# Optimization experiments

Measured on AMD Instinct MI355X. Metric: run time of the kernel, lower is better.

## Reference

```python
import jax, jax.numpy as jnp
import numpy as np

TIME_SCALE = 10.0
EPS = 1e-5


def _ln(x, g, b):
    m = jnp.mean(x, axis=-1, keepdims=True)
    v = jnp.mean((x - m) ** 2, axis=-1, keepdims=True)
    return (x - m) * jax.lax.rsqrt(v + EPS) * g + b


def setup_inputs() -> dict:
    key = jax.random.key(0)
    ks = jax.random.split(key, 16)
    B, S, D, H, C = 128, 2048, 67, 256, 1

    def lin(k, fan_in, shape):
        return (jax.random.uniform(k, shape, jnp.float32) * 2.0 - 1.0) / np.sqrt(fan_in)

    inp = {
        "x": jax.random.normal(ks[0], (B, S, D), jnp.float32),
        "dt": jax.random.uniform(ks[1], (B, S, 1), jnp.float32),
        # input LayerNorm
        "ln_in_g": jnp.ones((D,), jnp.float32),
        "ln_in_b": jnp.zeros((D,), jnp.float32),
        # feature projection: Linear(D,H) + LayerNorm(H) (+SiLU)
        "proj_W": lin(ks[2], D, (D, H)),
        "proj_b": jnp.zeros((H,), jnp.float32),
        "ln_p_g": jnp.ones((H,), jnp.float32),
        "ln_p_b": jnp.zeros((H,), jnp.float32),
        # CfC cell: four linears from concat([x_t, h]) (2H -> H)
        "W_ff1": lin(ks[3], 2 * H, (2 * H, H)),
        "b_ff1": jnp.zeros((H,), jnp.float32),
        "W_ff2": lin(ks[4], 2 * H, (2 * H, H)),
        "b_ff2": jnp.zeros((H,), jnp.float32),
        "W_ta": lin(ks[5], 2 * H, (2 * H, H)),
        "b_ta": jnp.zeros((H,), jnp.float32),
        "W_tb": lin(ks[6], 2 * H, (2 * H, H)),
        "b_tb": jnp.zeros((H,), jnp.float32),
        # event head: LayerNorm(H) + Linear(H, C)
        "head_g": jnp.ones((H,), jnp.float32),
        "head_b": jnp.zeros((H,), jnp.float32),
        "head_W": lin(ks[7], H, (H, C)),
        "head_bias": jnp.zeros((C,), jnp.float32),
    }
    return inp


def reference(x, dt, ln_in_g, ln_in_b, proj_W, proj_b, ln_p_g, ln_p_b,
              W_ff1, b_ff1, W_ff2, b_ff2, W_ta, b_ta, W_tb, b_tb,
              head_g, head_b, head_W, head_bias):
    B = x.shape[0]
    H = W_ff1.shape[1]

    xn = _ln(x, ln_in_g, ln_in_b)                      # [B,S,D]
    feat = jax.nn.silu(_ln(xn @ proj_W + proj_b, ln_p_g, ln_p_b))  # [B,S,H]

    xs = jnp.swapaxes(feat, 0, 1)                      # [S,B,H] time-major
    dts = jnp.swapaxes(dt * TIME_SCALE, 0, 1)          # [S,B,1]

    def step(h, inp):
        xt, dtt = inp
        z = jnp.concatenate([xt, h], axis=-1)          # [B,2H]
        ff1 = jnp.tanh(z @ W_ff1 + b_ff1)
        ff2 = jnp.tanh(z @ W_ff2 + b_ff2)
        t_interp = jax.nn.sigmoid((z @ W_ta + b_ta) * dtt + (z @ W_tb + b_tb))
        h_new = ff1 * (1.0 - t_interp) + t_interp * ff2
        return h_new, h_new

    h0 = jnp.zeros((B, H), x.dtype)
    _, hs = jax.lax.scan(step, h0, (xs, dts))          # hs: [S,B,H]
    seq = jnp.swapaxes(hs, 0, 1)                       # [B,S,H]
    logits = _ln(seq, head_g, head_b) @ head_W + head_bias  # [B,S,C]
    return logits
```

## Files before the change

kernel.cpp:

```cpp
#include <hip/hip_runtime.h>


typedef __bf16 bf16x8 __attribute__((ext_vector_type(8)));
typedef float f32x4 __attribute__((ext_vector_type(4)));
typedef int i32x4 __attribute__((ext_vector_type(4)));

#define DEVFN static __device__ __forceinline__

DEVFN float bf2f(unsigned short u){ return __uint_as_float(((unsigned)u) << 16); }
DEVFN unsigned short f2bf(float f){
  unsigned x = __float_as_uint(f);
  return (unsigned short)((x + 0x7FFFu + ((x >> 16) & 1u)) >> 16);
}
DEVFN float sigm(float x){ return 1.f / (1.f + __expf(-x)); }
DEVFN float tanh_f(float x){ return 1.f - 2.f / (__expf(2.f * x) + 1.f); }

#define GLD_LDS16(g, l) \
  __builtin_amdgcn_global_load_lds((const __attribute__((address_space(1))) void*)(g), \
                                   (__attribute__((address_space(3))) void*)(l), 16, 0, 0)

static constexpr int BB = 128;
static constexpr int SS = 2048;
static constexpr int DD = 67;

static constexpr size_t OFF_WXT   = 0;
static constexpr size_t OFF_WQ    = 524288;
static constexpr size_t OFF_SW    = 786432;
static constexpr size_t OFF_BIAS4 = 790528;
static constexpr size_t OFF_PWT   = 794624;
static constexpr size_t OFF_GW    = 843776;
static constexpr size_t OFF_SCAL  = 844800;
static constexpr size_t OFF_HST   = 845824;
static constexpr size_t OFF_FEAT  = 878592;

__global__ __launch_bounds__(256) void prep_kernel(
    const float* __restrict__ proj_W,
    const float* __restrict__ W_ff1, const float* __restrict__ b_ff1,
    const float* __restrict__ W_ff2, const float* __restrict__ b_ff2,
    const float* __restrict__ W_ta,  const float* __restrict__ b_ta,
    const float* __restrict__ W_tb,  const float* __restrict__ b_tb,
    const float* __restrict__ head_g, const float* __restrict__ head_b,
    const float* __restrict__ head_W, const float* __restrict__ head_bias,
    unsigned short* __restrict__ WxT, signed char* __restrict__ wq,
    float* __restrict__ sw, float* __restrict__ bias4,
    unsigned short* __restrict__ PWT, float* __restrict__ gW, float* __restrict__ scal)
{
  __shared__ float red[8];
  int bid = blockIdx.x, t = threadIdx.x;
  int wv = t >> 6, ln = t & 63;
  if (bid < 1024) {
    int J = bid, col = J & 255, which = J >> 8;
    const float* Wsrc = which == 0 ? W_ff1 : which == 1 ? W_ff2 : which == 2 ? W_ta : W_tb;
    const float* bsrc = which == 0 ? b_ff1 : which == 1 ? b_ff2 : which == 2 ? b_ta : b_tb;
    float w = Wsrc[t * 256 + col];
    WxT[J * 256 + t] = f2bf(w);
    if (t == 0) bias4[J] = bsrc[col];
  } else if (bid < 2048) {
    int J = bid - 1024, col = J & 255, which = J >> 8;
    const float* Wsrc = which == 0 ? W_ff1 : which == 1 ? W_ff2 : which == 2 ? W_ta : W_tb;
    float w = Wsrc[(256 + t) * 256 + col];
    float a = fabsf(w);
    for (int m = 32; m >= 1; m >>= 1) a = fmaxf(a, __shfl_xor(a, m, 64));
    if (ln == 0) red[wv] = a;
    __syncthreads();
    a = fmaxf(fmaxf(red[0], red[1]), fmaxf(red[2], red[3]));
    float scale = (a > 0.f) ? a * (1.f / 127.f) : 1.f;
    int q = (int)rintf(w / scale);
    q = q > 127 ? 127 : (q < -127 ? -127 : q);
    {
      int g = which, j = col, k = t;
      int wavw = j >> 5;
      int lane = ((k & 63) >> 4) * 16 + (j & 15);
      int tt = (j >> 4) & 1;
      int f = (g * 2 + tt) * 4 + (k >> 6);
      size_t dst = (size_t)(wavw * 64 + lane) * 512 + (size_t)f * 16 + (size_t)(k & 15);
      wq[dst] = (signed char)q;
    }
    if (t == 0) sw[J] = scale;
  } else {
    for (int idx = t; idx < 256 * 96; idx += 256) {
      int j = idx / 96, d = idx % 96;
      float v = (d < DD) ? proj_W[d * 256 + j] : 0.f;
      PWT[idx] = f2bf(v);
    }
    float gw = head_g[t] * head_W[t];
    gW[t] = gw;
    float bw = head_b[t] * head_W[t];
    float s1 = gw, s2 = bw;
    for (int m = 32; m >= 1; m >>= 1) { s1 += __shfl_xor(s1, m, 64); s2 += __shfl_xor(s2, m, 64); }
    if (ln == 0) { red[wv] = s1; red[4 + wv] = s2; }
    __syncthreads();
    if (t == 0) {
      scal[0] = red[0] + red[1] + red[2] + red[3];
      scal[1] = red[4] + red[5] + red[6] + red[7] + head_bias[0];
    }
  }
}

__global__ __launch_bounds__(512) void feat_kernel(
    const float* __restrict__ x, const float* __restrict__ ln_in_g, const float* __restrict__ ln_in_b,
    const float* __restrict__ proj_b, const float* __restrict__ ln_p_g, const float* __restrict__ ln_p_b,
    const unsigned short* __restrict__ PWT, unsigned short* __restrict__ feat,
    int s0, int C, int cshift)
{
  __shared__ __align__(16) unsigned short XA[64 * 104];
  __shared__ __align__(16) unsigned short XB[256 * 96];
  __shared__ float partS[64][4], partQ[64][4], statM[64], statI[64];
  int tid = threadIdx.x, w = tid >> 6, lane = tid & 63;
  int r0 = blockIdx.x * 64;

  {
    float g1v = (lane < 67) ? ln_in_g[lane] : 0.f;
    float b1v = (lane < 67) ? ln_in_b[lane] : 0.f;
    float g2v = (lane < 3) ? ln_in_g[64 + lane] : 0.f;
    float b2v = (lane < 3) ? ln_in_b[64 + lane] : 0.f;
    for (int i = 0; i < 8; ++i) {
      int rl = w * 8 + i;
      int r = r0 + rl;
      int bb = r >> cshift, cs = r & (C - 1);
      const float* xr = x + (size_t)(bb * SS + s0 + cs) * DD;
      float v0 = (lane < 67) ? xr[lane] : 0.f;
      float v1 = (lane < 3) ? xr[64 + lane] : 0.f;
      float s = v0 + v1, q = v0 * v0 + v1 * v1;
      for (int m = 32; m >= 1; m >>= 1) { s += __shfl_xor(s, m, 64); q += __shfl_xor(q, m, 64); }
      float mean = s * (1.f / 67.f);
      float var = q * (1.f / 67.f) - mean * mean;
      float inv = rsqrtf(var + 1e-5f);
      float xn0 = (v0 - mean) * inv * g1v + b1v;
      float xn1 = (v1 - mean) * inv * g2v + b2v;
      XA[rl * 104 + lane] = (lane < 67) ? f2bf(xn0) : (unsigned short)0;
      if (lane < 40) XA[rl * 104 + 64 + lane] = (lane < 3) ? f2bf(xn1) : (unsigned short)0;
    }
  }
  {
    const unsigned int* src = (const unsigned int*)PWT;
    unsigned int* dst = (unsigned int*)XB;
    for (int idx = tid; idx < 256 * 48; idx += 512) dst[idx] = src[idx];
  }
  __syncthreads();

  int wm = w >> 2, wn = w & 3;
  f32x4 acc[2][4];
  #pragma unroll
  for (int mt = 0; mt < 2; ++mt)
    #pragma unroll
    for (int nt = 0; nt < 4; ++nt) acc[mt][nt] = (f32x4){0.f, 0.f, 0.f, 0.f};
  #pragma unroll
  for (int ks = 0; ks < 3; ++ks) {
    int k = ks * 32 + (lane >> 4) * 8;
    bf16x8 a[2], b[4];
    #pragma unroll
    for (int mt = 0; mt < 2; ++mt) {
      int row = wm * 32 + mt * 16 + (lane & 15);
      a[mt] = *reinterpret_cast<const bf16x8*>(&XA[row * 104 + k]);
    }
    #pragma unroll
    for (int nt = 0; nt < 4; ++nt) {
      int col = wn * 64 + nt * 16 + (lane & 15);
      b[nt] = *reinterpret_cast<const bf16x8*>(&XB[col * 96 + k]);
    }
    #pragma unroll
    for (int mt = 0; mt < 2; ++mt)
      #pragma unroll
      for (int nt = 0; nt < 4; ++nt)
        acc[mt][nt] = __builtin_amdgcn_mfma_f32_16x16x32_bf16(a[mt], b[nt], acc[mt][nt], 0, 0, 0);
  }
  #pragma unroll
  for (int nt = 0; nt < 4; ++nt) {
    int col = wn * 64 + nt * 16 + (lane & 15);
    float pb = proj_b[col];
    #pragma unroll
    for (int mt = 0; mt < 2; ++mt)
      #pragma unroll
      for (int r = 0; r < 4; ++r) acc[mt][nt][r] += pb;
  }
  #pragma unroll
  for (int mt = 0; mt < 2; ++mt) {
    #pragma unroll
    for (int r = 0; r < 4; ++r) {
      float s = 0.f, q = 0.f;
      #pragma unroll
      for (int nt = 0; nt < 4; ++nt) { float v = acc[mt][nt][r]; s += v; q += v * v; }
      for (int m = 1; m < 16; m <<= 1) { s += __shfl_xor(s, m, 16); q += __shfl_xor(q, m, 16); }
      if ((lane & 15) == 0) {
        int row = wm * 32 + mt * 16 + (lane >> 4) * 4 + r;
        partS[row][wn] = s; partQ[row][wn] = q;
      }
    }
  }
  __syncthreads();
  if (tid < 64) {
    float s = partS[tid][0] + partS[tid][1] + partS[tid][2] + partS[tid][3];
    float q = partQ[tid][0] + partQ[tid][1] + partQ[tid][2] + partQ[tid][3];
    float mean = s * (1.f / 256.f);
    float var = q * (1.f / 256.f) - mean * mean;
    statM[tid] = mean; statI[tid] = rsqrtf(var + 1e-5f);
  }
  __syncthreads();
  #pragma unroll
  for (int nt = 0; nt < 4; ++nt) {
    int col = wn * 64 + nt * 16 + (lane & 15);
    float gc = ln_p_g[col], bc = ln_p_b[col];
    #pragma unroll
    for (int mt = 0; mt < 2; ++mt)
      #pragma unroll
      for (int r = 0; r < 4; ++r) {
        int row = wm * 32 + mt * 16 + (lane >> 4) * 4 + r;
        float v = acc[mt][nt][r];
        float y = (v - statM[row]) * statI[row] * gc + bc;
        float sl = y * sigm(y);
        feat[(size_t)(r0 + row) * 256 + col] = f2bf(sl);
      }
  }
}

__global__ __launch_bounds__(256, 2) void gemm_kernel(
    const unsigned short* __restrict__ feat, const unsigned short* __restrict__ WxT,
    const float* __restrict__ bias4, unsigned short* __restrict__ pre)
{
  __shared__ __align__(16) unsigned short Abuf[128 * 64];
  __shared__ __align__(16) unsigned short Bbuf[128 * 64];
  int tid = threadIdx.x, w = tid >> 6, lane = tid & 63;
  int m0 = blockIdx.x * 128, n0 = blockIdx.y * 128;
  int wm = w >> 1, wn = w & 1;
  f32x4 acc[4][4];
  #pragma unroll
  for (int i = 0; i < 4; ++i)
    #pragma unroll
    for (int j = 0; j < 4; ++j) acc[i][j] = (f32x4){0.f, 0.f, 0.f, 0.f};

  #pragma unroll 1
  for (int ks = 0; ks < 4; ++ks) {
    int k0 = ks * 64;
    #pragma unroll
    for (int i = 0; i < 4; ++i) {
      int c = i * 256 + tid;
      int row = c >> 3, cc = c & 7;
      const unsigned short* ga = feat + (size_t)(m0 + row) * 256 + (k0 + cc * 8);
      const unsigned short* gb = WxT + (size_t)(n0 + row) * 256 + (k0 + cc * 8);
      char* la = (char*)Abuf + (size_t)(i * 256 + w * 64) * 16;
      char* lb = (char*)Bbuf + (size_t)(i * 256 + w * 64) * 16;
      GLD_LDS16(ga, la);
      GLD_LDS16(gb, lb);
    }
    __syncthreads();
    #pragma unroll
    for (int kk = 0; kk < 2; ++kk) {
      int k = kk * 32 + (lane >> 4) * 8;
      bf16x8 a[4], b[4];
      #pragma unroll
      for (int mt = 0; mt < 4; ++mt) {
        int row = wm * 64 + mt * 16 + (lane & 15);
        a[mt] = *reinterpret_cast<const bf16x8*>(&Abuf[row * 64 + k]);
      }
      #pragma unroll
      for (int nt = 0; nt < 4; ++nt) {
        int col = wn * 64 + nt * 16 + (lane & 15);
        b[nt] = *reinterpret_cast<const bf16x8*>(&Bbuf[col * 64 + k]);
      }
      #pragma unroll
      for (int mt = 0; mt < 4; ++mt)
        #pragma unroll
        for (int nt = 0; nt < 4; ++nt)
          acc[mt][nt] = __builtin_amdgcn_mfma_f32_16x16x32_bf16(a[mt], b[nt], acc[mt][nt], 0, 0, 0);
    }
    __syncthreads();
  }
  #pragma unroll
  for (int nt = 0; nt < 4; ++nt) {
    int col = n0 + wn * 64 + nt * 16 + (lane & 15);
    float bv = bias4[col];
    #pragma unroll
    for (int mt = 0; mt < 4; ++mt)
      #pragma unroll
      for (int r = 0; r < 4; ++r) {
        int row = m0 + wm * 64 + mt * 16 + (lane >> 4) * 4 + r;
        pre[(size_t)row * 1024 + col] = f2bf(acc[mt][nt][r] + bv);
      }
  }
}

#define WRA(n, val) asm volatile("v_accvgpr_write_b32 a" #n ", %0" :: "v"(val) : "a" #n)
#define WR4(n0,n1,n2,n3, q) \
  do { WRA(n0,(q).x); WRA(n1,(q).y); WRA(n2,(q).z); WRA(n3,(q).w); } while (0)
#define MFMA_AB(acc, af, b0, b1) \
  asm volatile("v_mfma_i32_16x16x64_i8 %0, %1, a[" #b0 ":" #b1 "], %2" \
               : "=&v"(acc) : "v"(af), "v"(acc))

__global__ __attribute__((amdgpu_flat_work_group_size(512, 512)))
           __attribute__((amdgpu_waves_per_eu(2, 2)))
void scan_kernel(
    const unsigned short* __restrict__ pre, const float* __restrict__ dt,
    const signed char* __restrict__ wq, const float* __restrict__ sw,
    int* __restrict__ hstate, unsigned short* __restrict__ hseq, int s0, int C)
{
  __shared__ __align__(16) signed char hq2[2][256];
  int tid = threadIdx.x, w = tid >> 6, l = tid & 63;
  int b = blockIdx.x;

  {
    const int4* wp = (const int4*)(wq + (size_t)tid * 512);
    int4 q0, q1, q2, q3, q4, q5, q6, q7;
    q0=wp[0]; q1=wp[1]; q2=wp[2]; q3=wp[3]; q4=wp[4]; q5=wp[5]; q6=wp[6]; q7=wp[7];
    WR4(0,1,2,3,q0);     WR4(4,5,6,7,q1);     WR4(8,9,10,11,q2);    WR4(12,13,14,15,q3);
    WR4(16,17,18,19,q4); WR4(20,21,22,23,q5); WR4(24,25,26,27,q6);  WR4(28,29,30,31,q7);
    q0=wp[8]; q1=wp[9]; q2=wp[10]; q3=wp[11]; q4=wp[12]; q5=wp[13]; q6=wp[14]; q7=wp[15];
    WR4(32,33,34,35,q0); WR4(36,37,38,39,q1); WR4(40,41,42,43,q2);  WR4(44,45,46,47,q3);
    WR4(48,49,50,51,q4); WR4(52,53,54,55,q5); WR4(56,57,58,59,q6);  WR4(60,61,62,63,q7);
    q0=wp[16]; q1=wp[17]; q2=wp[18]; q3=wp[19]; q4=wp[20]; q5=wp[21]; q6=wp[22]; q7=wp[23];
    WR4(64,65,66,67,q0); WR4(68,69,70,71,q1); WR4(72,73,74,75,q2);  WR4(76,77,78,79,q3);
    WR4(80,81,82,83,q4); WR4(84,85,86,87,q5); WR4(88,89,90,91,q6);  WR4(92,93,94,95,q7);
    q0=wp[24]; q1=wp[25]; q2=wp[26]; q3=wp[27]; q4=wp[28]; q5=wp[29]; q6=wp[30]; q7=wp[31];
    WR4(96,97,98,99,q0);   WR4(100,101,102,103,q1); WR4(104,105,106,107,q2); WR4(108,109,110,111,q3);
    WR4(112,113,114,115,q4); WR4(116,117,118,119,q5); WR4(120,121,122,123,q6); WR4(124,125,126,127,q7);
  }

  int lg = l >> 4;
  int tt = lg & 1;
  bool gact = (lg < 2);
  int j = w * 32 + tt * 16 + (l & 15);

  float sc0 = 0.f, sc1 = 0.f, sc2 = 0.f, sc3 = 0.f;
  unsigned short pu0 = 0, pu1 = 0, pu2 = 0, pu3 = 0;
  float dtc = 0.f;
  const unsigned short* preB = pre + (size_t)b * C * 1024;
  unsigned short* hsB = hseq + (size_t)b * C * 256;
  if (gact) {
    sc0 = sw[j]       * (1.f / 127.f);
    sc1 = sw[256 + j] * (1.f / 127.f);
    sc2 = sw[512 + j] * (1.f / 127.f);
    sc3 = sw[768 + j] * (1.f / 127.f);
    pu0 = preB[j]; pu1 = preB[256 + j]; pu2 = preB[512 + j]; pu3 = preB[768 + j];
    dtc = dt[b * SS + s0] * 10.f;
  }

  if (tid < 64) ((int*)hq2[0])[tid] = (s0 == 0) ? 0 : hstate[b * 64 + tid];
  int cur = 0;
  __syncthreads();

  for (int cs = 0; cs < C; ++cs) {
    const signed char* hb = hq2[cur];
    int aoff = lg << 4;
    i32x4 A0 = *reinterpret_cast<const i32x4*>(hb + 0 * 64 + aoff);
    i32x4 A1 = *reinterpret_cast<const i32x4*>(hb + 1 * 64 + aoff);
    i32x4 A2 = *reinterpret_cast<const i32x4*>(hb + 2 * 64 + aoff);
    i32x4 A3 = *reinterpret_cast<const i32x4*>(hb + 3 * 64 + aoff);
    i32x4 c0 = {0,0,0,0}, c1 = {0,0,0,0}, c2 = {0,0,0,0}, c3 = {0,0,0,0};
    i32x4 c4 = {0,0,0,0}, c5 = {0,0,0,0}, c6 = {0,0,0,0}, c7 = {0,0,0,0};
    MFMA_AB(c0, A0,   0,   3); MFMA_AB(c1, A0,  16,  19); MFMA_AB(c2, A0,  32,  35); MFMA_AB(c3, A0,  48,  51);
    MFMA_AB(c4, A0,  64,  67); MFMA_AB(c5, A0,  80,  83); MFMA_AB(c6, A0,  96,  99); MFMA_AB(c7, A0, 112, 115);
    MFMA_AB(c0, A1,   4,   7); MFMA_AB(c1, A1,  20,  23); MFMA_AB(c2, A1,  36,  39); MFMA_AB(c3, A1,  52,  55);
    MFMA_AB(c4, A1,  68,  71); MFMA_AB(c5, A1,  84,  87); MFMA_AB(c6, A1, 100, 103); MFMA_AB(c7, A1, 116, 119);
    MFMA_AB(c0, A2,   8,  11); MFMA_AB(c1, A2,  24,  27); MFMA_AB(c2, A2,  40,  43); MFMA_AB(c3, A2,  56,  59);
    MFMA_AB(c4, A2,  72,  75); MFMA_AB(c5, A2,  88,  91); MFMA_AB(c6, A2, 104, 107); MFMA_AB(c7, A2, 120, 123);
    MFMA_AB(c0, A3,  12,  15); MFMA_AB(c1, A3,  28,  31); MFMA_AB(c2, A3,  44,  47); MFMA_AB(c3, A3,  60,  63);
    MFMA_AB(c4, A3,  76,  79); MFMA_AB(c5, A3,  92,  95); MFMA_AB(c6, A3, 108, 111); MFMA_AB(c7, A3, 124, 127);
    asm volatile("s_nop 7\n\ts_nop 7\n\ts_nop 7");
    if (gact) {
      int d0 = tt ? c1.x : c0.x;
      int d1 = tt ? c3.x : c2.x;
      int d2 = tt ? c5.x : c4.x;
      int d3 = tt ? c7.x : c6.x;
      float g0 = (float)d0 * sc0 + bf2f(pu0);
      float g1 = (float)d1 * sc1 + bf2f(pu1);
      float g2 = (float)d2 * sc2 + bf2f(pu2);
      float g3 = (float)d3 * sc3 + bf2f(pu3);
      float f1 = tanh_f(g0), f2 = tanh_f(g1);
      float ti = sigm(g2 * dtc + g3);
      float h = f1 + ti * (f2 - f1);
      int q = (int)rintf(h * 127.f);
      q = q > 127 ? 127 : (q < -127 ? -127 : q);
      hq2[cur ^ 1][j] = (signed char)q;
      hsB[(size_t)cs * 256 + j] = f2bf(h);
      if (cs + 1 < C) {
        const unsigned short* pn = preB + (size_t)(cs + 1) * 1024;
        pu0 = pn[j]; pu1 = pn[256 + j]; pu2 = pn[512 + j]; pu3 = pn[768 + j];
        dtc = dt[b * SS + s0 + cs + 1] * 10.f;
      }
    }
    cur ^= 1;
    __syncthreads();
  }
  if (tid < 64) hstate[b * 64 + tid] = ((const int*)hq2[cur])[tid];
}

__global__ __launch_bounds__(256) void head_kernel(
    const unsigned short* __restrict__ hseq, const float* __restrict__ gW,
    const float* __restrict__ scal, float* __restrict__ out, int s0, int C, int cshift)
{
  int tid = threadIdx.x, wv = tid >> 6, l = tid & 63;
  int row = blockIdx.x * 4 + wv;
  const unsigned short* hr = hseq + (size_t)row * 256 + l * 4;
  ushort4 u = *reinterpret_cast<const ushort4*>(hr);
  float4 gw = *reinterpret_cast<const float4*>(gW + l * 4);
  float v0 = bf2f(u.x), v1 = bf2f(u.y), v2 = bf2f(u.z), v3 = bf2f(u.w);
  float s1 = v0 + v1 + v2 + v3;
  float s2 = v0 * v0 + v1 * v1 + v2 * v2 + v3 * v3;
  float s3 = v0 * gw.x + v1 * gw.y + v2 * gw.z + v3 * gw.w;
  for (int m = 32; m >= 1; m >>= 1) {
    s1 += __shfl_xor(s1, m, 64); s2 += __shfl_xor(s2, m, 64); s3 += __shfl_xor(s3, m, 64);
  }
  if (l == 0) {
    float mean = s1 * (1.f / 256.f);
    float var = s2 * (1.f / 256.f) - mean * mean;
    float inv = rsqrtf(var + 1e-5f);
    int b = row >> cshift, cs = row & (C - 1);
    out[(size_t)b * SS + s0 + cs] = inv * (s3 - mean * scal[0]) + scal[1];
  }
}

extern "C" void kernel_launch(void* const* d_in, const int* in_sizes, int n_in,
                              void* d_out, int out_size, void* d_ws, size_t ws_size,
                              hipStream_t stream)
{
  (void)in_sizes; (void)n_in; (void)out_size;
  const float* x        = (const float*)d_in[0];
  const float* dt       = (const float*)d_in[1];
  const float* ln_in_g  = (const float*)d_in[2];
  const float* ln_in_b  = (const float*)d_in[3];
  const float* proj_W   = (const float*)d_in[4];
  const float* proj_b   = (const float*)d_in[5];
  const float* ln_p_g   = (const float*)d_in[6];
  const float* ln_p_b   = (const float*)d_in[7];
  const float* W_ff1    = (const float*)d_in[8];
  const float* b_ff1    = (const float*)d_in[9];
  const float* W_ff2    = (const float*)d_in[10];
  const float* b_ff2    = (const float*)d_in[11];
  const float* W_ta     = (const float*)d_in[12];
  const float* b_ta     = (const float*)d_in[13];
  const float* W_tb     = (const float*)d_in[14];
  const float* b_tb     = (const float*)d_in[15];
  const float* head_g   = (const float*)d_in[16];
  const float* head_b   = (const float*)d_in[17];
  const float* head_W   = (const float*)d_in[18];
  const float* head_bias= (const float*)d_in[19];

  char* ws = (char*)d_ws;
  unsigned short* WxT = (unsigned short*)(ws + OFF_WXT);
  signed char* wq     = (signed char*)(ws + OFF_WQ);
  float* sw           = (float*)(ws + OFF_SW);
  float* bias4        = (float*)(ws + OFF_BIAS4);
  unsigned short* PWT = (unsigned short*)(ws + OFF_PWT);
  float* gWv          = (float*)(ws + OFF_GW);
  float* scal         = (float*)(ws + OFF_SCAL);
  int* hstate         = (int*)(ws + OFF_HST);

  int C = 16;
  for (int c = 2048; c >= 16; c >>= 1) {
    size_t need = OFF_FEAT + (size_t)c * 65536 + (size_t)c * 262144;
    if (need <= ws_size) { C = c; break; }
  }
  unsigned short* featb = (unsigned short*)(ws + OFF_FEAT);
  unsigned short* preb  = (unsigned short*)(ws + OFF_FEAT + (size_t)C * 65536);
  int cshift = 31 - __builtin_clz((unsigned)C);

  prep_kernel<<<2049, 256, 0, stream>>>(proj_W, W_ff1, b_ff1, W_ff2, b_ff2, W_ta, b_ta, W_tb, b_tb,
                                        head_g, head_b, head_W, head_bias,
                                        WxT, wq, sw, bias4, PWT, gWv, scal);
  int nch = SS / C;
  for (int ch = 0; ch < nch; ++ch) {
    int s0 = ch * C;
    feat_kernel<<<dim3(BB * C / 64), 512, 0, stream>>>(x, ln_in_g, ln_in_b, proj_b, ln_p_g, ln_p_b,
                                                       PWT, featb, s0, C, cshift);
    gemm_kernel<<<dim3(BB * C / 128, 8), 256, 0, stream>>>(featb, WxT, bias4, preb);
    scan_kernel<<<dim3(BB), 512, 0, stream>>>(preb, dt, wq, sw, hstate, featb, s0, C);
    head_kernel<<<dim3(BB * C / 4), 256, 0, stream>>>(featb, gWv, scal, (float*)d_out, s0, C, cshift);
  }
}
```

Before: 2.569 ms.

## Batch 16 sequences per scan block with staged pre-activations in LDS

The recurrent scan now processes 16 batch rows per workgroup instead of one, so all 16 rows of each MFMA tile carry real work rather than only the first. The GEMM writes pre-activations in a time-major, batch-grouped layout, and the scan double-buffers each step's slice into swizzled LDS using global-to-LDS loads. dt for the chunk is preloaded into LDS, and the chunk size is capped at 512. The launch drops from 128 to 8 workgroups, which leaves far fewer blocks to keep the GPU busy in exchange for better MFMA use per step.

```diff
diff --git a/kernel.cpp b/kernel.cpp
--- a/kernel.cpp
+++ b/kernel.cpp
@@ -216,7 +216,8 @@
 
 __global__ __launch_bounds__(256, 2) void gemm_kernel(
     const unsigned short* __restrict__ feat, const unsigned short* __restrict__ WxT,
-    const float* __restrict__ bias4, unsigned short* __restrict__ pre)
+    const float* __restrict__ bias4, unsigned short* __restrict__ pre,
+    int C, int cshift)
 {
   __shared__ __align__(16) unsigned short Abuf[128 * 64];
   __shared__ __align__(16) unsigned short Bbuf[128 * 64];
@@ -268,14 +269,16 @@
   }
   #pragma unroll
   for (int nt = 0; nt < 4; ++nt) {
-    int col = n0 + wn * 64 + nt * 16 + (lane & 15);
-    float bv = bias4[col];
+    int colJ = n0 + wn * 64 + nt * 16 + (lane & 15);
+    float bv = bias4[colJ];
     #pragma unroll
     for (int mt = 0; mt < 4; ++mt)
       #pragma unroll
       for (int r = 0; r < 4; ++r) {
         int row = m0 + wm * 64 + mt * 16 + (lane >> 4) * 4 + r;
-        pre[(size_t)row * 1024 + col] = f2bf(acc[mt][nt][r] + bv);
+        int bb = row >> cshift, cs2 = row & (C - 1);
+        int bgy = bb >> 4, bl = bb & 15;
+        pre[(((size_t)bgy * C + cs2) * 16 + bl) * 1024 + colJ] = f2bf(acc[mt][nt][r] + bv);
       }
   }
 }
@@ -290,13 +293,17 @@
 __global__ __attribute__((amdgpu_flat_work_group_size(512, 512)))
            __attribute__((amdgpu_waves_per_eu(2, 2)))
 void scan_kernel(
-    const unsigned short* __restrict__ pre, const float* __restrict__ dt,
+    const unsigned short* __restrict__ pre2, const float* __restrict__ dt,
     const signed char* __restrict__ wq, const float* __restrict__ sw,
-    int* __restrict__ hstate, unsigned short* __restrict__ hseq, int s0, int C)
+    int* __restrict__ hstate, unsigned short* __restrict__ hseq,
+    int s0, int C, int cshift)
 {
-  __shared__ __align__(16) signed char hq2[2][256];
+  __shared__ __align__(16) signed char h_lds[2][16][256];
+  __shared__ __align__(16) unsigned short preT[2][16][1024];
+  __shared__ float dt_lds[16 * 512];
   int tid = threadIdx.x, w = tid >> 6, l = tid & 63;
-  int b = blockIdx.x;
+  int bg = blockIdx.x;
+  int lg = l >> 4, c = l & 15;
 
   {
     const int4* wp = (const int4*)(wq + (size_t)tid * 512);
@@ -315,36 +322,64 @@
     WR4(112,113,114,115,q4); WR4(116,117,118,119,q5); WR4(120,121,122,123,q6); WR4(124,125,126,127,q7);
   }
 
-  int lg = l >> 4;
-  int tt = lg & 1;
-  bool gact = (lg < 2);
-  int j = w * 32 + tt * 16 + (l & 15);
-
-  float sc0 = 0.f, sc1 = 0.f, sc2 = 0.f, sc3 = 0.f;
-  unsigned short pu0 = 0, pu1 = 0, pu2 = 0, pu3 = 0;
-  float dtc = 0.f;
-  const unsigned short* preB = pre + (size_t)b * C * 1024;
-  unsigned short* hsB = hseq + (size_t)b * C * 256;
-  if (gact) {
-    sc0 = sw[j]       * (1.f / 127.f);
-    sc1 = sw[256 + j] * (1.f / 127.f);
-    sc2 = sw[512 + j] * (1.f / 127.f);
-    sc3 = sw[768 + j] * (1.f / 127.f);
-    pu0 = preB[j]; pu1 = preB[256 + j]; pu2 = preB[512 + j]; pu3 = preB[768 + j];
-    dtc = dt[b * SS + s0] * 10.f;
-  }
-
-  if (tid < 64) ((int*)hq2[0])[tid] = (s0 == 0) ? 0 : hstate[b * 64 + tid];
+  float sc[2][4];
+  #pragma unroll
+  for (int tt = 0; tt < 2; ++tt)
+    #pragma unroll
+    for (int g = 0; g < 4; ++g)
+      sc[tt][g] = sw[g * 256 + w * 32 + tt * 16 + c] * (1.f / 127.f);
+
+  for (int idx = tid; idx < 16 * C; idx += 512) {
+    int bl = idx >> cshift, cs2 = idx & (C - 1);
+    dt_lds[idx] = dt[(size_t)(bg * 16 + bl) * SS + s0 + cs2] * 10.f;
+  }
+  if (s0 == 0) {
+    for (int idx = tid; idx < 1024; idx += 512) ((int*)&h_lds[0][0][0])[idx] = 0;
+  } else if (tid < 256) {
+    int bl = tid >> 4, blk = tid & 15;
+    int4 v = *(const int4*)&hstate[(bg * 16 + bl) * 64 + blk * 4];
+    *(int4*)&h_lds[0][bl][(blk * 16) ^ ((bl & 7) << 4)] = v;
+  }
+
+  const unsigned short* preB2 = pre2 + (size_t)bg * C * 16384;
+  int soff0, soff1, soff2, soff3;
+  {
+    int g16, bl, jb;
+    g16 = w * 256 + 0 * 64 + l; bl = g16 >> 7; jb = g16 & 127; soff0 = bl * 1024 + (jb ^ (bl & 7)) * 8;
+    g16 = w * 256 + 1 * 64 + l; bl = g16 >> 7; jb = g16 & 127; soff1 = bl * 1024 + (jb ^ (bl & 7)) * 8;
+    g16 = w * 256 + 2 * 64 + l; bl = g16 >> 7; jb = g16 & 127; soff2 = bl * 1024 + (jb ^ (bl & 7)) * 8;
+    g16 = w * 256 + 3 * 64 + l; bl = g16 >> 7; jb = g16 & 127; soff3 = bl * 1024 + (jb ^ (bl & 7)) * 8;
+  }
+#define STAGE_PRE(cs_t, buf) do { \
+    const unsigned short* _s = preB2 + (size_t)(cs_t) * 16384; \
+    char* _d = (char*)&preT[0][0][0] + (buf) * 32768 + w * 4096; \
+    GLD_LDS16(_s + soff0, _d); \
+    GLD_LDS16(_s + soff1, _d + 1024); \
+    GLD_LDS16(_s + soff2, _d + 2048); \
+    GLD_LDS16(_s + soff3, _d + 3072); \
+  } while (0)
+
+  int aswz = (c & 7) << 4;
+  int ab = c * 256;
+  int ak0 = ab + ((lg * 16 +   0) ^ aswz);
+  int ak1 = ab + ((lg * 16 +  64) ^ aswz);
+  int ak2 = ab + ((lg * 16 + 128) ^ aswz);
+  int ak3 = ab + ((lg * 16 + 192) ^ aswz);
+
+  STAGE_PRE(0, 0);
+  asm volatile("s_waitcnt vmcnt(0)" ::: "memory");
+  __syncthreads();
+
   int cur = 0;
-  __syncthreads();
-
   for (int cs = 0; cs < C; ++cs) {
-    const signed char* hb = hq2[cur];
-    int aoff = lg << 4;
-    i32x4 A0 = *reinterpret_cast<const i32x4*>(hb + 0 * 64 + aoff);
-    i32x4 A1 = *reinterpret_cast<const i32x4*>(hb + 1 * 64 + aoff);
-    i32x4 A2 = *reinterpret_cast<const i32x4*>(hb + 2 * 64 + aoff);
-    i32x4 A3 = *reinterpret_cast<const i32x4*>(hb + 3 * 64 + aoff);
+    int nxt = cur ^ 1;
+    const signed char* hb = &h_lds[0][0][0] + cur * 4096;
+    i32x4 A0 = *(const i32x4*)(hb + ak0);
+    i32x4 A1 = *(const i32x4*)(hb + ak1);
+    i32x4 A2 = *(const i32x4*)(hb + ak2);
+    i32x4 A3 = *(const i32x4*)(hb + ak3);
+    if (cs + 1 < C) STAGE_PRE(cs + 1, nxt);
+
     i32x4 c0 = {0,0,0,0}, c1 = {0,0,0,0}, c2 = {0,0,0,0}, c3 = {0,0,0,0};
     i32x4 c4 = {0,0,0,0}, c5 = {0,0,0,0}, c6 = {0,0,0,0}, c7 = {0,0,0,0};
     MFMA_AB(c0, A0,   0,   3); MFMA_AB(c1, A0,  16,  19); MFMA_AB(c2, A0,  32,  35); MFMA_AB(c3, A0,  48,  51);
@@ -356,32 +391,48 @@
     MFMA_AB(c0, A3,  12,  15); MFMA_AB(c1, A3,  28,  31); MFMA_AB(c2, A3,  44,  47); MFMA_AB(c3, A3,  60,  63);
     MFMA_AB(c4, A3,  76,  79); MFMA_AB(c5, A3,  92,  95); MFMA_AB(c6, A3, 108, 111); MFMA_AB(c7, A3, 124, 127);
     asm volatile("s_nop 7\n\ts_nop 7\n\ts_nop 7");
-    if (gact) {
-      int d0 = tt ? c1.x : c0.x;
-      int d1 = tt ? c3.x : c2.x;
-      int d2 = tt ? c5.x : c4.x;
-      int d3 = tt ? c7.x : c6.x;
-      float g0 = (float)d0 * sc0 + bf2f(pu0);
-      float g1 = (float)d1 * sc1 + bf2f(pu1);
-      float g2 = (float)d2 * sc2 + bf2f(pu2);
-      float g3 = (float)d3 * sc3 + bf2f(pu3);
-      float f1 = tanh_f(g0), f2 = tanh_f(g1);
-      float ti = sigm(g2 * dtc + g3);
-      float h = f1 + ti * (f2 - f1);
-      int q = (int)rintf(h * 127.f);
-      q = q > 127 ? 127 : (q < -127 ? -127 : q);
-      hq2[cur ^ 1][j] = (signed char)q;
-      hsB[(size_t)cs * 256 + j] = f2bf(h);
-      if (cs + 1 < C) {
-        const unsigned short* pn = preB + (size_t)(cs + 1) * 1024;
-        pu0 = pn[j]; pu1 = pn[256 + j]; pu2 = pn[512 + j]; pu3 = pn[768 + j];
-        dtc = dt[b * SS + s0 + cs + 1] * 10.f;
+
+    float dtv[4];
+    #pragma unroll
+    for (int r = 0; r < 4; ++r) dtv[r] = dt_lds[((lg * 4 + r) << cshift) + cs];
+
+    #pragma unroll
+    for (int tt = 0; tt < 2; ++tt) {
+      int j = w * 32 + tt * 16 + c;
+      #pragma unroll
+      for (int r = 0; r < 4; ++r) {
+        int bl = lg * 4 + r;
+        int jx = j ^ ((bl & 7) << 3);
+        float p0 = bf2f(preT[cur][bl][jx]);
+        float p1 = bf2f(preT[cur][bl][256 + jx]);
+        float p2 = bf2f(preT[cur][bl][512 + jx]);
+        float p3 = bf2f(preT[cur][bl][768 + jx]);
+        int d0 = tt ? c1[r] : c0[r];
+        int d1 = tt ? c3[r] : c2[r];
+        int d2 = tt ? c5[r] : c4[r];
+        int d3 = tt ? c7[r] : c6[r];
+        float g0 = (float)d0 * sc[tt][0] + p0;
+        float g1 = (float)d1 * sc[tt][1] + p1;
+        float g2 = (float)d2 * sc[tt][2] + p2;
+        float g3 = (float)d3 * sc[tt][3] + p3;
+        float f1v = tanh_f(g0), f2v = tanh_f(g1);
+        float ti = sigm(g2 * dtv[r] + g3);
+        float h = f1v + ti * (f2v - f1v);
+        int q = (int)rintf(h * 127.f);
+        q = q > 127 ? 127 : (q < -127 ? -127 : q);
+        h_lds[nxt][bl][j ^ ((bl & 7) << 4)] = (signed char)q;
+        hseq[((size_t)(bg * 16 + bl) * C + cs) * 256 + j] = f2bf(h);
       }
     }
-    cur ^= 1;
+    asm volatile("s_waitcnt vmcnt(8)" ::: "memory");
+    cur = nxt;
     __syncthreads();
   }
-  if (tid < 64) hstate[b * 64 + tid] = ((const int*)hq2[cur])[tid];
+  if (tid < 256) {
+    int bl = tid >> 4, blk = tid & 15;
+    int4 v = *(const int4*)&h_lds[cur][bl][(blk * 16) ^ ((bl & 7) << 4)];
+    *(int4*)&hstate[(bg * 16 + bl) * 64 + blk * 4] = v;
+  }
 }
 
 __global__ __launch_bounds__(256) void head_kernel(
@@ -446,7 +497,7 @@
   int* hstate         = (int*)(ws + OFF_HST);
 
   int C = 16;
-  for (int c = 2048; c >= 16; c >>= 1) {
+  for (int c = 512; c >= 16; c >>= 1) {
     size_t need = OFF_FEAT + (size_t)c * 65536 + (size_t)c * 262144;
     if (need <= ws_size) { C = c; break; }
   }
@@ -462,8 +513,8 @@
     int s0 = ch * C;
     feat_kernel<<<dim3(BB * C / 64), 512, 0, stream>>>(x, ln_in_g, ln_in_b, proj_b, ln_p_g, ln_p_b,
                                                        PWT, featb, s0, C, cshift);
-    gemm_kernel<<<dim3(BB * C / 128, 8), 256, 0, stream>>>(featb, WxT, bias4, preb);
-    scan_kernel<<<dim3(BB), 512, 0, stream>>>(preb, dt, wq, sw, hstate, featb, s0, C);
+    gemm_kernel<<<dim3(BB * C / 128, 8), 256, 0, stream>>>(featb, WxT, bias4, preb, C, cshift);
+    scan_kernel<<<dim3(BB / 16), 512, 0, stream>>>(preb, dt, wq, sw, hstate, featb, s0, C, cshift);
     head_kernel<<<dim3(BB * C / 4), 256, 0, stream>>>(featb, gWv, scal, (float*)d_out, s0, C, cshift);
   }
 }
```

Measured after the change: 5.982 ms. 2.33x slower.
